# Kernel tuning notes

Measured on AMD Instinct MI355X. Metric: run time of the kernel, lower is better.

## Reference

```python
import jax, jax.numpy as jnp
import numpy as np

C, H, W = 16, 260, 346   # time bins, sensor height, sensor width (DAVIS346)
N = 16_000_000           # number of events
NUM_VOX = 2 * C * H * W  # B=1, two polarities


def setup_inputs() -> dict:
    key = jax.random.key(0)
    kx, ky, kt, kp = jax.random.split(key, 4)
    x = jax.random.randint(kx, (N,), 0, W).astype(jnp.float32)
    y = jax.random.randint(ky, (N,), 0, H).astype(jnp.float32)
    t = jax.random.uniform(kt, (N,), minval=1e-6, maxval=1.0)
    p = (2 * jax.random.randint(kp, (N,), 0, 2) - 1).astype(jnp.float32)  # {-1, 1}
    events = jnp.stack([x, y, t, p], axis=1)  # [N, 4]
    return {"events": events}


def reference(events):
    x, y, t, p_raw = events.T  # each [N]
    # per-batch t normalization (B=1; batch id read from last column == 0)
    m = p_raw == 0
    tmax = jnp.max(jnp.where(m, t, -jnp.inf))
    t = jnp.where(m & jnp.any(m), t / tmax, t)
    p = (p_raw + 1) * 0.5          # {-1,1} -> {0,1}
    b = 0.0                        # single sample, batch offset 0
    # bin i such that i/C < t <= (i+1)/C  <=>  i = ceil(t*C) - 1
    i_bin = jnp.ceil(t * C) - 1.0
    valid = (t > 0.0) & (t <= 1.0)
    idx = x + W * y + W * H * C * p + W * H * C * 2 * b + W * H * i_bin
    idx = jnp.where(valid, idx, float(NUM_VOX)).astype(jnp.int32)  # sentinel -> dropped
    vox = jnp.zeros((NUM_VOX,), dtype=events.dtype)
    vox = vox.at[idx].set(1.0, mode="drop")  # non-accumulating scatter (put_)
    return vox.reshape(-1, 2, C, H, W)
```

## Files before the change

kernel.cpp:

```cpp
#include <hip/hip_runtime.h>


#define CBINS 16
#define HDIM  260
#define WDIM  346
#define NVOX  (2 * CBINS * HDIM * WDIM)
#define NBUCK 256
#define RGN   11264
#define CHUNK 7424
#define CAP   131072u
#define SENT  0xFFFFFFFFu

typedef float fvec4 __attribute__((ext_vector_type(4)));

__device__ __forceinline__ unsigned ev_to_packed(fvec4 e) {
    float t = e.z;
    if (!(t > 0.f && t <= 1.f)) return SENT;
    float bin = __builtin_ceilf(t * 16.f) - 1.f;
    float bp  = (e.w > 0.f) ? (bin + 16.f) : bin;
    float idxf = __builtin_fmaf(346.f, e.y, e.x);
    idxf = __builtin_fmaf(89960.f, bp, idxf);
    unsigned idx = (unsigned)idxf;
    unsigned b = idx / (unsigned)RGN;
    return (b << 16) | (idx - b * (unsigned)RGN);
}

__global__ __launch_bounds__(256) void partition_kernel(
        const fvec4* __restrict__ ev, int n,
        unsigned short* __restrict__ seg,
        unsigned* __restrict__ gcur) {
    __shared__ unsigned       raw[CHUNK];
    __shared__ unsigned short srt[CHUNK];
    __shared__ unsigned hist4[4][NBUCK];
    __shared__ unsigned bnd[NBUCK];
    __shared__ unsigned lenA[NBUCK];
    __shared__ unsigned cursor[NBUCK];
    __shared__ unsigned sbase[NBUCK];
    __shared__ unsigned wsum[4];

    const int w = blockIdx.x, tid = threadIdx.x;
    const int wave = tid >> 6, lane = tid & 63;
    const int base = w * CHUNK;
    const int nev = min(CHUNK, n - base);

    hist4[0][tid >> 2 | ((tid & 3) << 6)] = 0;
    hist4[1][tid] = 0; hist4[2][tid] = 0; hist4[3][tid] = 0;
    hist4[0][tid] = 0;
    __syncthreads();

    unsigned* myh = hist4[wave];
    int k = tid;
    for (; k + 768 < nev; k += 1024) {
        fvec4 e0 = __builtin_nontemporal_load(&ev[base + k]);
        fvec4 e1 = __builtin_nontemporal_load(&ev[base + k + 256]);
        fvec4 e2 = __builtin_nontemporal_load(&ev[base + k + 512]);
        fvec4 e3 = __builtin_nontemporal_load(&ev[base + k + 768]);
        unsigned i0 = ev_to_packed(e0), i1 = ev_to_packed(e1);
        unsigned i2 = ev_to_packed(e2), i3 = ev_to_packed(e3);
        raw[k]       = i0; raw[k + 256] = i1;
        raw[k + 512] = i2; raw[k + 768] = i3;
        if (i0 != SENT) atomicAdd(&myh[i0 >> 16], 1u);
        if (i1 != SENT) atomicAdd(&myh[i1 >> 16], 1u);
        if (i2 != SENT) atomicAdd(&myh[i2 >> 16], 1u);
        if (i3 != SENT) atomicAdd(&myh[i3 >> 16], 1u);
    }
    for (; k < nev; k += 256) {
        unsigned i0 = ev_to_packed(__builtin_nontemporal_load(&ev[base + k]));
        raw[k] = i0;
        if (i0 != SENT) atomicAdd(&myh[i0 >> 16], 1u);
    }
    __syncthreads();

    unsigned val = hist4[0][tid] + hist4[1][tid] + hist4[2][tid] + hist4[3][tid];
    unsigned incl = val;
    #pragma unroll
    for (int s = 1; s < 64; s <<= 1) {
        unsigned u = __shfl_up(incl, s, 64);
        if (lane >= s) incl += u;
    }
    if (lane == 63) wsum[wave] = incl;
    __syncthreads();
    unsigned off = 0;
    if (wave > 0) off += wsum[0];
    if (wave > 1) off += wsum[1];
    if (wave > 2) off += wsum[2];
    unsigned excl = incl - val + off;
    bnd[tid]  = excl;
    lenA[tid] = val;
    cursor[tid] = excl;
    sbase[tid] = atomicAdd(&gcur[tid], (val + 31u) & ~31u);
    __syncthreads();

    for (k = tid; k < nev; k += 256) {
        unsigned vv = raw[k];
        if (vv != SENT) {
            unsigned pos = atomicAdd(&cursor[vv >> 16], 1u);
            srt[pos] = (unsigned short)(vv & 0xFFFFu);
        }
    }
    __syncthreads();

    for (int b = wave; b < NBUCK; b += 4) {
        unsigned s   = bnd[b], len = lenA[b];
        unsigned gb  = sbase[b];
        unsigned plen = (len + 31u) & ~31u;
        unsigned short* dst = seg + (size_t)b * CAP + gb;
        for (unsigned j = lane; j < plen; j += 64)
            dst[j] = (j < len) ? srt[s + j] : (unsigned short)RGN;
    }
}

__global__ __launch_bounds__(1024) void build_kernel(
        const unsigned short* __restrict__ seg,
        const unsigned* __restrict__ gcur,
        fvec4* __restrict__ out) {
    __shared__ unsigned char flag[12288];
    const int b = blockIdx.x, tid = threadIdx.x;

    for (int i = tid; i < 12288 / 4; i += 1024) ((unsigned*)flag)[i] = 0;
    __syncthreads();

    unsigned n_b = min(gcur[b], CAP);
    const unsigned* p32 = (const unsigned*)(seg + (size_t)b * CAP);
    for (unsigned j = tid; j < n_b / 2; j += 1024) {
        unsigned v = __builtin_nontemporal_load(&p32[j]);
        flag[v & 0xFFFFu] = 1;
        flag[v >> 16]     = 1;
    }
    __syncthreads();

    for (int i = tid; i < RGN / 4; i += 1024) {
        int g = b * (RGN / 4) + i;
        if (g < NVOX / 4) {
            uchar4 f = ((const uchar4*)flag)[i];
            fvec4 vv = { f.x ? 1.f : 0.f, f.y ? 1.f : 0.f,
                         f.z ? 1.f : 0.f, f.w ? 1.f : 0.f };
            __builtin_nontemporal_store(vv, &out[g]);
        }
    }
}

__global__ __launch_bounds__(256) void scatter_flags(const fvec4* __restrict__ ev,
                                                     unsigned char* __restrict__ flags,
                                                     int n) {
    int i = blockIdx.x * blockDim.x + threadIdx.x;
    if (i >= n) return;
    fvec4 e = __builtin_nontemporal_load(&ev[i]);
    float t = e.z;
    if (t > 0.f && t <= 1.f) {
        int xi = (int)e.x, yi = (int)e.y;
        int pi = (e.w > 0.f) ? 1 : 0;
        int bin = (int)ceilf(t * (float)CBINS) - 1;
        flags[xi + WDIM * yi + WDIM * HDIM * (bin + CBINS * pi)] = 1;
    }
}
__global__ __launch_bounds__(256) void expand_flags(const uchar4* __restrict__ flags,
                                                    fvec4* __restrict__ out, int n4) {
    int i = blockIdx.x * blockDim.x + threadIdx.x;
    if (i >= n4) return;
    uchar4 f = flags[i];
    fvec4 v = { f.x ? 1.f : 0.f, f.y ? 1.f : 0.f, f.z ? 1.f : 0.f, f.w ? 1.f : 0.f };
    __builtin_nontemporal_store(v, &out[i]);
}

extern "C" void kernel_launch(void* const* d_in, const int* in_sizes, int n_in,
                              void* d_out, int out_size, void* d_ws, size_t ws_size,
                              hipStream_t stream) {
    const fvec4* ev = (const fvec4*)d_in[0];
    int n  = in_sizes[0] / 4;
    int n4 = out_size / 4;
    int nchunk = (n + CHUNK - 1) / CHUNK;

    size_t seg_bytes = (size_t)NBUCK * CAP * sizeof(unsigned short);
    size_t cur_bytes = NBUCK * sizeof(unsigned);

    if (ws_size >= seg_bytes + cur_bytes) {
        unsigned short* seg = (unsigned short*)d_ws;
        unsigned* gcur = (unsigned*)((char*)d_ws + seg_bytes);
        hipMemsetAsync(gcur, 0, cur_bytes, stream);
        partition_kernel<<<nchunk, 256, 0, stream>>>(ev, n, seg, gcur);
        build_kernel<<<NBUCK, 1024, 0, stream>>>(seg, gcur, (fvec4*)d_out);
    } else {
        unsigned char* flags = (unsigned char*)d_ws;
        hipMemsetAsync(flags, 0, NVOX, stream);
        scatter_flags<<<(n + 255) / 256, 256, 0, stream>>>(ev, flags, n);
        expand_flags<<<(n4 + 255) / 256, 256, 0, stream>>>((const uchar4*)flags,
                                                           (fvec4*)d_out, n4);
    }
}
```

Before: 388.4 us.

## Replace per-chunk histogram+scan bucket sort with fixed-slot slabs and global overflow

The partition kernel no longer does the two-pass local counting sort (histogram, prefix scan, scatter). Each event is appended directly into a fixed 64-slot shared slab per bucket, and excess entries spill to a global overflow list that a new fixup kernel writes into the output afterwards. This cuts LDS traffic and barriers, and per-bucket segment capacity now scales with chunk count. It adds a third kernel launch and global atomics on the overflow counter. With about 29 events per bucket per chunk on average, overflow should be rare.

```diff
diff --git a/kernel.cpp b/kernel.cpp
--- a/kernel.cpp
+++ b/kernel.cpp
@@ -8,7 +8,7 @@
 #define NBUCK 256
 #define RGN   11264
 #define CHUNK 7424
-#define CAP   131072u
+#define LCAP  64
 #define SENT  0xFFFFFFFFu
 
 typedef float fvec4 __attribute__((ext_vector_type(4)));
@@ -28,100 +28,83 @@
 __global__ __launch_bounds__(256) void partition_kernel(
         const fvec4* __restrict__ ev, int n,
         unsigned short* __restrict__ seg,
-        unsigned* __restrict__ gcur) {
-    __shared__ unsigned       raw[CHUNK];
-    __shared__ unsigned short srt[CHUNK];
-    __shared__ unsigned hist4[4][NBUCK];
-    __shared__ unsigned bnd[NBUCK];
-    __shared__ unsigned lenA[NBUCK];
-    __shared__ unsigned cursor[NBUCK];
+        unsigned* __restrict__ gcur,
+        unsigned* __restrict__ ovf,
+        unsigned cap, unsigned ovf_cap) {
+    __shared__ unsigned short slab[NBUCK * LCAP];
+    __shared__ unsigned cnt[NBUCK];
     __shared__ unsigned sbase[NBUCK];
-    __shared__ unsigned wsum[4];
 
     const int w = blockIdx.x, tid = threadIdx.x;
     const int wave = tid >> 6, lane = tid & 63;
     const int base = w * CHUNK;
     const int nev = min(CHUNK, n - base);
 
-    hist4[0][tid >> 2 | ((tid & 3) << 6)] = 0;
-    hist4[1][tid] = 0; hist4[2][tid] = 0; hist4[3][tid] = 0;
-    hist4[0][tid] = 0;
+    cnt[tid] = 0;
     __syncthreads();
 
-    unsigned* myh = hist4[wave];
     int k = tid;
     for (; k + 768 < nev; k += 1024) {
         fvec4 e0 = __builtin_nontemporal_load(&ev[base + k]);
         fvec4 e1 = __builtin_nontemporal_load(&ev[base + k + 256]);
         fvec4 e2 = __builtin_nontemporal_load(&ev[base + k + 512]);
         fvec4 e3 = __builtin_nontemporal_load(&ev[base + k + 768]);
-        unsigned i0 = ev_to_packed(e0), i1 = ev_to_packed(e1);
-        unsigned i2 = ev_to_packed(e2), i3 = ev_to_packed(e3);
-        raw[k]       = i0; raw[k + 256] = i1;
-        raw[k + 512] = i2; raw[k + 768] = i3;
-        if (i0 != SENT) atomicAdd(&myh[i0 >> 16], 1u);
-        if (i1 != SENT) atomicAdd(&myh[i1 >> 16], 1u);
-        if (i2 != SENT) atomicAdd(&myh[i2 >> 16], 1u);
-        if (i3 != SENT) atomicAdd(&myh[i3 >> 16], 1u);
+        unsigned pk[4] = { ev_to_packed(e0), ev_to_packed(e1),
+                           ev_to_packed(e2), ev_to_packed(e3) };
+        #pragma unroll
+        for (int q = 0; q < 4; ++q) {
+            unsigned v = pk[q];
+            if (v == SENT) continue;
+            unsigned b = v >> 16;
+            unsigned slot = atomicAdd(&cnt[b], 1u);
+            if (slot < LCAP) slab[b * LCAP + slot] = (unsigned short)v;
+            else {
+                unsigned pos = atomicAdd(&ovf[0], 1u);
+                if (pos < ovf_cap) ovf[1 + pos] = b * (unsigned)RGN + (v & 0xFFFFu);
+            }
+        }
     }
     for (; k < nev; k += 256) {
-        unsigned i0 = ev_to_packed(__builtin_nontemporal_load(&ev[base + k]));
-        raw[k] = i0;
-        if (i0 != SENT) atomicAdd(&myh[i0 >> 16], 1u);
-    }
-    __syncthreads();
-
-    unsigned val = hist4[0][tid] + hist4[1][tid] + hist4[2][tid] + hist4[3][tid];
-    unsigned incl = val;
-    #pragma unroll
-    for (int s = 1; s < 64; s <<= 1) {
-        unsigned u = __shfl_up(incl, s, 64);
-        if (lane >= s) incl += u;
-    }
-    if (lane == 63) wsum[wave] = incl;
-    __syncthreads();
-    unsigned off = 0;
-    if (wave > 0) off += wsum[0];
-    if (wave > 1) off += wsum[1];
-    if (wave > 2) off += wsum[2];
-    unsigned excl = incl - val + off;
-    bnd[tid]  = excl;
-    lenA[tid] = val;
-    cursor[tid] = excl;
-    sbase[tid] = atomicAdd(&gcur[tid], (val + 31u) & ~31u);
-    __syncthreads();
-
-    for (k = tid; k < nev; k += 256) {
-        unsigned vv = raw[k];
-        if (vv != SENT) {
-            unsigned pos = atomicAdd(&cursor[vv >> 16], 1u);
-            srt[pos] = (unsigned short)(vv & 0xFFFFu);
+        unsigned v = ev_to_packed(__builtin_nontemporal_load(&ev[base + k]));
+        if (v == SENT) continue;
+        unsigned b = v >> 16;
+        unsigned slot = atomicAdd(&cnt[b], 1u);
+        if (slot < LCAP) slab[b * LCAP + slot] = (unsigned short)v;
+        else {
+            unsigned pos = atomicAdd(&ovf[0], 1u);
+            if (pos < ovf_cap) ovf[1 + pos] = b * (unsigned)RGN + (v & 0xFFFFu);
         }
     }
     __syncthreads();
 
+    {
+        unsigned len  = min(cnt[tid], (unsigned)LCAP);
+        unsigned plen = (len + 31u) & ~31u;
+        sbase[tid] = atomicAdd(&gcur[tid], plen);
+    }
+    __syncthreads();
+
     for (int b = wave; b < NBUCK; b += 4) {
-        unsigned s   = bnd[b], len = lenA[b];
-        unsigned gb  = sbase[b];
+        unsigned len  = min(cnt[b], (unsigned)LCAP);
         unsigned plen = (len + 31u) & ~31u;
-        unsigned short* dst = seg + (size_t)b * CAP + gb;
+        unsigned short* dst = seg + (size_t)b * cap + sbase[b];
         for (unsigned j = lane; j < plen; j += 64)
-            dst[j] = (j < len) ? srt[s + j] : (unsigned short)RGN;
+            dst[j] = (j < len) ? slab[b * LCAP + j] : (unsigned short)RGN;
     }
 }
 
 __global__ __launch_bounds__(1024) void build_kernel(
         const unsigned short* __restrict__ seg,
         const unsigned* __restrict__ gcur,
-        fvec4* __restrict__ out) {
+        fvec4* __restrict__ out, unsigned cap) {
     __shared__ unsigned char flag[12288];
     const int b = blockIdx.x, tid = threadIdx.x;
 
     for (int i = tid; i < 12288 / 4; i += 1024) ((unsigned*)flag)[i] = 0;
     __syncthreads();
 
-    unsigned n_b = min(gcur[b], CAP);
-    const unsigned* p32 = (const unsigned*)(seg + (size_t)b * CAP);
+    unsigned n_b = min(gcur[b], cap);
+    const unsigned* p32 = (const unsigned*)(seg + (size_t)b * cap);
     for (unsigned j = tid; j < n_b / 2; j += 1024) {
         unsigned v = __builtin_nontemporal_load(&p32[j]);
         flag[v & 0xFFFFu] = 1;
@@ -138,6 +121,15 @@
             __builtin_nontemporal_store(vv, &out[g]);
         }
     }
+}
+
+__global__ __launch_bounds__(256) void fixup_kernel(const unsigned* __restrict__ ovf,
+                                                    float* __restrict__ out,
+                                                    unsigned ovf_cap) {
+    unsigned cnt = min(ovf[0], ovf_cap);
+    for (unsigned j = blockIdx.x * blockDim.x + threadIdx.x; j < cnt;
+         j += gridDim.x * blockDim.x)
+        out[ovf[1 + j]] = 1.0f;
 }
 
 __global__ __launch_bounds__(256) void scatter_flags(const fvec4* __restrict__ ev,
@@ -171,15 +163,20 @@
     int n4 = out_size / 4;
     int nchunk = (n + CHUNK - 1) / CHUNK;
 
-    size_t seg_bytes = (size_t)NBUCK * CAP * sizeof(unsigned short);
+    unsigned cap = (unsigned)nchunk * LCAP;
+    unsigned ovf_cap = (unsigned)n;
+    size_t seg_bytes = (size_t)NBUCK * cap * sizeof(unsigned short);
     size_t cur_bytes = NBUCK * sizeof(unsigned);
+    size_t ovf_bytes = (size_t)(1 + ovf_cap) * sizeof(unsigned);
 
-    if (ws_size >= seg_bytes + cur_bytes) {
+    if (ws_size >= seg_bytes + cur_bytes + ovf_bytes) {
         unsigned short* seg = (unsigned short*)d_ws;
         unsigned* gcur = (unsigned*)((char*)d_ws + seg_bytes);
-        hipMemsetAsync(gcur, 0, cur_bytes, stream);
-        partition_kernel<<<nchunk, 256, 0, stream>>>(ev, n, seg, gcur);
-        build_kernel<<<NBUCK, 1024, 0, stream>>>(seg, gcur, (fvec4*)d_out);
+        unsigned* ovf  = gcur + NBUCK;
+        hipMemsetAsync(gcur, 0, (NBUCK + 1) * sizeof(unsigned), stream);
+        partition_kernel<<<nchunk, 256, 0, stream>>>(ev, n, seg, gcur, ovf, cap, ovf_cap);
+        build_kernel<<<NBUCK, 1024, 0, stream>>>(seg, gcur, (fvec4*)d_out, cap);
+        fixup_kernel<<<64, 256, 0, stream>>>(ovf, (float*)d_out, ovf_cap);
     } else {
         unsigned char* flags = (unsigned char*)d_ws;
         hipMemsetAsync(flags, 0, NVOX, stream);
```

After: 381.2 us. No clear change (-1.8%).
